# Kernel tuning notes

Measured on AMD Instinct MI355X. Metric: run time of the kernel, lower is better.

## Reference

```python
import jax, jax.numpy as jnp
import numpy as np

EPS = 1e-5

def _bn_relu(y, mean, var, scale, bias):
    # y: (b, c, n); eval-mode batchnorm over channel axis, then ReLU
    inv = scale / jnp.sqrt(var + EPS)
    return jax.nn.relu((y - mean[None, :, None]) * inv[None, :, None] + bias[None, :, None])

def setup_inputs() -> dict:
    key = jax.random.key(0)
    ks = jax.random.split(key, 6)
    b, c, n, cr = 4, 256, 4096, 32
    inp = {
        'x': jax.random.normal(ks[0], (b, c, n), jnp.float32),
        'w_q': jax.random.normal(ks[1], (cr, c), jnp.float32) * (1.0 / np.sqrt(c)),
        'w_k': jax.random.normal(ks[2], (cr, c), jnp.float32) * (1.0 / np.sqrt(c)),
        'w_v': jax.random.normal(ks[3], (c, c), jnp.float32) * (1.0 / np.sqrt(c)),
        'bn1_scale': jnp.ones((cr,), jnp.float32), 'bn1_bias': jnp.zeros((cr,), jnp.float32),
        'bn1_mean': jnp.zeros((cr,), jnp.float32), 'bn1_var': jnp.ones((cr,), jnp.float32),
        'bn2_scale': jnp.ones((cr,), jnp.float32), 'bn2_bias': jnp.zeros((cr,), jnp.float32),
        'bn2_mean': jnp.zeros((cr,), jnp.float32), 'bn2_var': jnp.ones((cr,), jnp.float32),
        'bn3_scale': jnp.ones((c,), jnp.float32), 'bn3_bias': jnp.zeros((c,), jnp.float32),
        'bn3_mean': jnp.zeros((c,), jnp.float32), 'bn3_var': jnp.ones((c,), jnp.float32),
        'gamma': jax.random.normal(ks[4], (1,), jnp.float32),
    }
    return inp

def reference(x, w_q, w_k, w_v,
              bn1_scale, bn1_bias, bn1_mean, bn1_var,
              bn2_scale, bn2_bias, bn2_mean, bn2_var,
              bn3_scale, bn3_bias, bn3_mean, bn3_var,
              gamma):
    # x: (b, c, n). Original views as (b, c, n, 1) so width=1, height=n.
    b, c, n = x.shape
    # 1x1 conv == channel matmul, then BN+ReLU
    q = _bn_relu(jnp.einsum('oc,bcn->bon', w_q, x), bn1_mean, bn1_var, bn1_scale, bn1_bias)  # (b, c', n)
    k = _bn_relu(jnp.einsum('oc,bcn->bon', w_k, x), bn2_mean, bn2_var, bn2_scale, bn2_bias)  # (b, c', n)
    v = _bn_relu(jnp.einsum('oc,bcn->bon', w_v, x), bn3_mean, bn3_var, bn3_scale, bn3_bias)  # (b, c, n)
    # energy_H: (b, n, n) with -inf diagonal (self-attention along 'height')
    energy_h = jnp.einsum('bdi,bdj->bij', q, k)
    eye = jnp.eye(n, dtype=bool)
    energy_h = jnp.where(eye[None], -jnp.inf, energy_h)
    # energy_W: width=1 -> per-position self energy (b, n)
    energy_w = jnp.sum(q * k, axis=1)
    # softmax over concat of n H-logits and 1 W-logit
    att = jax.nn.softmax(jnp.concatenate([energy_h, energy_w[..., None]], axis=-1), axis=-1)  # (b, n, n+1)
    att_h = att[..., :n]        # (b, n, n), query i -> key j
    att_w = att[..., n]         # (b, n)
    out_h = jnp.einsum('bcj,bij->bci', v, att_h)   # aggregate values along height
    out_w = v * att_w[:, None, :]                  # width=1 self term
    out = gamma[0] * (out_h + out_w) + x
    return out
```

## Files before the change

kernel.cpp:

```cpp
#include <hip/hip_runtime.h>

#define Bb 4
#define Cc 256
#define Nn 4096
#define CR 32
#define EPS_BN 1e-5f
#define SHIFT2 28.853900817779268f
#define LOG2E  1.4426950408889634f
#define JSPLIT 4
#define JSL (Nn / JSPLIT)
#define TJ 64
#define NTILES (JSL / TJ)

typedef __attribute__((ext_vector_type(8))) short short8;
typedef __attribute__((ext_vector_type(4))) float f32x4;

__device__ inline unsigned int pk2(float a, float b) {
    __bf16 ha = (__bf16)a, hb = (__bf16)b;
    unsigned short ra = __builtin_bit_cast(unsigned short, ha);
    unsigned short rb = __builtin_bit_cast(unsigned short, hb);
    return ((unsigned int)rb << 16) | ra;
}
__device__ inline float blo(unsigned int u) { return __uint_as_float(u << 16); }
__device__ inline float bhi(unsigned int u) { return __uint_as_float(u & 0xffff0000u); }
__device__ inline float ex2(float x) { return __builtin_amdgcn_exp2f(x); }

__global__ __launch_bounds__(256) void prep_w(
    const float* __restrict__ wq, const float* __restrict__ wk,
    const float* __restrict__ wv, __bf16* __restrict__ Wf)
{
    const int r16 = blockIdx.x;
    const int tid = threadIdx.x;
#pragma unroll
    for (int ss = 0; ss < 2; ++ss) {
        int s = tid + ss * 256;
        int kc = s >> 6, lane = s & 63;
        int R = r16 * 16 + (lane & 15);
        const float* src = (R < 32) ? (wq + (size_t)R * Cc)
                         : (R < 64) ? (wk + (size_t)(R - 32) * Cc)
                                    : (wv + (size_t)(R - 64) * Cc);
        const float* p = src + kc * 32 + (lane >> 4) * 8;
        float4 a = *(const float4*)p;
        float4 c2 = *(const float4*)(p + 4);
        uint4 pk = { pk2(a.x,a.y), pk2(a.z,a.w), pk2(c2.x,c2.y), pk2(c2.z,c2.w) };
        *(uint4*)&Wf[(((size_t)r16 * 8 + kc) * 64 + lane) * 8] = pk;
    }
}

__global__ __launch_bounds__(256) void qkv_kernel(
    const float* __restrict__ x, const __bf16* __restrict__ Wf,
    const float* __restrict__ bn1s, const float* __restrict__ bn1b, const float* __restrict__ bn1m, const float* __restrict__ bn1v,
    const float* __restrict__ bn2s, const float* __restrict__ bn2b, const float* __restrict__ bn2m, const float* __restrict__ bn2v,
    const float* __restrict__ bn3s, const float* __restrict__ bn3b, const float* __restrict__ bn3m, const float* __restrict__ bn3v,
    __bf16* __restrict__ Qt, __bf16* __restrict__ Kt, __bf16* __restrict__ Vb)
{
    __shared__ __align__(16) float  sXf[4][32 * 40];
    __shared__ __align__(16) __bf16 sXt[4][2][32 * 40];
    __shared__ __align__(16) __bf16 oT[128 * 136];

    const int tid = threadIdx.x;
    const int n0 = blockIdx.x * 128, g = blockIdx.y, b = blockIdx.z;
    const int lane = tid & 63, w = tid >> 6;
    const int l15 = lane & 15, l4 = lane >> 4;
    const int nmt = (g == 0) ? 4 : 8;
    const int r16b = (g == 0) ? 0 : 4 + (g - 1) * 8;

    float*  sXfw  = &sXf[w][0];
    __bf16* sXtw0 = &sXt[w][0][0];
    __bf16* sXtw1 = &sXt[w][1][0];

    const int cr = lane >> 3, nq = lane & 7;
    const float* xbase = x + (size_t)(b * Cc + cr) * Nn + n0 + w * 32 + nq * 4;

    float4 xg[4];
#pragma unroll
    for (int it = 0; it < 4; ++it)
        xg[it] = *(const float4*)&xbase[(size_t)(it * 8) * Nn];

    f32x4 acc[8][2];
#pragma unroll
    for (int mt = 0; mt < 8; ++mt)
#pragma unroll
        for (int nt = 0; nt < 2; ++nt) acc[mt][nt] = (f32x4){0.f, 0.f, 0.f, 0.f};

    for (int kc = 0; kc < 8; ++kc) {
#pragma unroll
        for (int it = 0; it < 4; ++it)
            *(float4*)&sXfw[(it * 8 + cr) * 40 + nq * 4] = xg[it];

        if (kc + 1 < 8) {
#pragma unroll
            for (int it = 0; it < 4; ++it)
                xg[it] = *(const float4*)&xbase[(size_t)((kc + 1) * 32 + it * 8) * Nn];
        }

#pragma unroll
        for (int s = 0; s < 2; ++s) {
            int n = lane & 31, c0 = (lane >> 5) * 8 + s * 16;
            float h[8], lo[8];
#pragma unroll
            for (int j = 0; j < 8; ++j) {
                float v = sXfw[(c0 + j) * 40 + n];
                float hh = (float)(__bf16)v;
                h[j] = hh; lo[j] = v - hh;
            }
            uint4 H = { pk2(h[0],h[1]), pk2(h[2],h[3]), pk2(h[4],h[5]), pk2(h[6],h[7]) };
            uint4 L = { pk2(lo[0],lo[1]), pk2(lo[2],lo[3]), pk2(lo[4],lo[5]), pk2(lo[6],lo[7]) };
            *(uint4*)&sXtw0[n * 40 + c0] = H;
            *(uint4*)&sXtw1[n * 40 + c0] = L;
        }

        short8 bh[2], bl[2];
#pragma unroll
        for (int nt = 0; nt < 2; ++nt) {
            bh[nt] = *(const short8*)&sXtw0[(nt * 16 + l15) * 40 + l4 * 8];
            bl[nt] = *(const short8*)&sXtw1[(nt * 16 + l15) * 40 + l4 * 8];
        }
        short8 af[8];
#pragma unroll
        for (int mt = 0; mt < 8; ++mt)
            if (mt < nmt)
                af[mt] = *(const short8*)&Wf[(((size_t)(r16b + mt) * 8 + kc) * 64 + lane) * 8];
#pragma unroll
        for (int mt = 0; mt < 8; ++mt) {
            if (mt < nmt) {
#pragma unroll
                for (int nt = 0; nt < 2; ++nt) {
                    acc[mt][nt] = __builtin_amdgcn_mfma_f32_16x16x32_bf16(af[mt], bh[nt], acc[mt][nt], 0, 0, 0);
                    acc[mt][nt] = __builtin_amdgcn_mfma_f32_16x16x32_bf16(af[mt], bl[nt], acc[mt][nt], 0, 0, 0);
                }
            }
        }
    }

    if (g == 0) {
#pragma unroll
        for (int mt = 0; mt < 4; ++mt) {
            float scl[4], off[4];
#pragma unroll
            for (int r = 0; r < 4; ++r) {
                int R = mt * 16 + l4 * 4 + r;
                float s, o;
                if (R < 32) {
                    s = bn1s[R] * __frsqrt_rn(bn1v[R] + EPS_BN);
                    o = bn1b[R] - bn1m[R] * s;
                } else {
                    int row = R - 32;
                    s = bn2s[row] * __frsqrt_rn(bn2v[row] + EPS_BN);
                    o = bn2b[row] - bn2m[row] * s;
                    s *= LOG2E; o *= LOG2E;
                }
                scl[r] = s; off[r] = o;
            }
            __bf16* dst = (mt < 2) ? Qt : Kt;
            int d0 = (mt & 1) * 16 + l4 * 4;
#pragma unroll
            for (int nt = 0; nt < 2; ++nt) {
                f32x4 a = acc[mt][nt];
                float e0 = fmaxf(fmaf(a.x, scl[0], off[0]), 0.f);
                float e1 = fmaxf(fmaf(a.y, scl[1], off[1]), 0.f);
                float e2 = fmaxf(fmaf(a.z, scl[2], off[2]), 0.f);
                float e3 = fmaxf(fmaf(a.w, scl[3], off[3]), 0.f);
                uint2 p = { pk2(e0, e1), pk2(e2, e3) };
                int n = n0 + w * 32 + nt * 16 + l15;
                *(uint2*)&dst[(size_t)(b * Nn + n) * CR + d0] = p;
            }
        }
    } else {
        const int vr0 = (g - 1) * 128;
#pragma unroll
        for (int mt = 0; mt < 8; ++mt) {
            float scl[4], off[4];
#pragma unroll
            for (int r = 0; r < 4; ++r) {
                int row = vr0 + mt * 16 + l4 * 4 + r;
                float s = bn3s[row] * __frsqrt_rn(bn3v[row] + EPS_BN);
                scl[r] = s; off[r] = bn3b[row] - bn3m[row] * s;
            }
#pragma unroll
            for (int nt = 0; nt < 2; ++nt) {
                f32x4 a = acc[mt][nt];
                float e[4];
                e[0] = fmaxf(fmaf(a.x, scl[0], off[0]), 0.f);
                e[1] = fmaxf(fmaf(a.y, scl[1], off[1]), 0.f);
                e[2] = fmaxf(fmaf(a.z, scl[2], off[2]), 0.f);
                e[3] = fmaxf(fmaf(a.w, scl[3], off[3]), 0.f);
                int ncol = w * 32 + nt * 16 + l15;
#pragma unroll
                for (int r = 0; r < 4; ++r)
                    oT[(mt * 16 + l4 * 4 + r) * 136 + ncol] = (__bf16)e[r];
            }
        }
        __syncthreads();
        int rr = tid >> 1, qq = tid & 1;
        size_t vrow = (size_t)(b * Cc + vr0 + rr) * Nn + n0 + qq * 64;
#pragma unroll
        for (int e8 = 0; e8 < 8; ++e8)
            *(uint4*)&Vb[vrow + e8 * 8] = *(const uint4*)&oT[rr * 136 + qq * 64 + e8 * 8];
    }
}

__global__ __launch_bounds__(256, 4) void attn_kernel(
    const __bf16* __restrict__ Qt, const __bf16* __restrict__ Kt,
    const __bf16* __restrict__ Vb,
    __bf16* __restrict__ PO, float* __restrict__ PL)
{
    __shared__ __align__(16) __bf16 sQ[64 * 40];
    __shared__ __align__(16) __bf16 sP[64 * 72];
    __shared__ __align__(16) float  sL[4][64];

    const int tid = threadIdx.x, lane = tid & 63, w = tid >> 6;
    const int b = blockIdx.z, iblk = blockIdx.x;
    const int js = blockIdx.y & 3, ch = blockIdx.y >> 2;
    const int i0 = iblk * 64, cb = ch * 128;
    const int l15 = lane & 15, l4 = lane >> 4;

    {
        int i = tid >> 2, o = tid & 3;
        *(uint4*)&sQ[i * 40 + o * 8] =
            *(const uint4*)&Qt[(size_t)(b * Nn + i0 + i) * CR + o * 8];
    }
    __syncthreads();
    short8 qf[4];
#pragma unroll
    for (int it = 0; it < 4; ++it)
        qf[it] = *(const short8*)&sQ[(it * 16 + l15) * 40 + l4 * 8];

    f32x4 oacc[8];
#pragma unroll
    for (int z = 0; z < 8; ++z) oacc[z] = (f32x4){0.f, 0.f, 0.f, 0.f};
    float lp[4] = {0.f, 0.f, 0.f, 0.f};

    const size_t jb = (size_t)js * JSL;
    short8 kf = *(const short8*)&Kt[(size_t)(b * Nn + jb + 16 * w + l15) * CR + l4 * 8];

    const __bf16* vrow0 = Vb + (size_t)(b * Cc + cb + w * 32 + l15) * Nn;

    for (int t = 0; t < NTILES; ++t) {
        const size_t j0 = jb + (size_t)t * TJ;

        short8 vf[4];
#pragma unroll
        for (int u = 0; u < 4; ++u) {
            int jh = u >> 1, ct = u & 1;
            vf[u] = *(const short8*)&vrow0[(size_t)(ct * 16) * Nn + j0 + jh * 32 + l4 * 8];
        }

#pragma unroll
        for (int it = 0; it < 4; ++it) {
            f32x4 c0 = (f32x4){0.f, 0.f, 0.f, 0.f};
            c0 = __builtin_amdgcn_mfma_f32_16x16x32_bf16(kf, qf[it], c0, 0, 0, 0);
            float e0 = ex2(c0.x - SHIFT2);
            float e1 = ex2(c0.y - SHIFT2);
            float e2 = ex2(c0.z - SHIFT2);
            float e3 = ex2(c0.w - SHIFT2);
            lp[it] += (e0 + e1) + (e2 + e3);
            uint2 p2 = { pk2(e0, e1), pk2(e2, e3) };
            *(uint2*)&sP[(it * 16 + l15) * 72 + w * 16 + l4 * 4] = p2;
        }
        __syncthreads();

        if (t + 1 < NTILES)
            kf = *(const short8*)&Kt[(size_t)(b * Nn + j0 + TJ + 16 * w + l15) * CR + l4 * 8];

        __builtin_amdgcn_s_setprio(1);
#pragma unroll
        for (int jh = 0; jh < 2; ++jh) {
            short8 pf[4];
#pragma unroll
            for (int it = 0; it < 4; ++it)
                pf[it] = *(const short8*)&sP[(it * 16 + l15) * 72 + jh * 32 + l4 * 8];
#pragma unroll
            for (int ct = 0; ct < 2; ++ct) {
#pragma unroll
                for (int it = 0; it < 4; ++it)
                    oacc[it * 2 + ct] = __builtin_amdgcn_mfma_f32_16x16x32_bf16(
                        pf[it], vf[jh * 2 + ct], oacc[it * 2 + ct], 0, 0, 0);
            }
        }
        __builtin_amdgcn_s_setprio(0);
        __syncthreads();
    }

#pragma unroll
    for (int it = 0; it < 4; ++it) {
        float v = lp[it];
        v += __shfl_xor(v, 16);
        v += __shfl_xor(v, 32);
        if (lane < 16) sL[w][it * 16 + lane] = v;
    }
    __syncthreads();
    if (ch == 0 && tid < 64)
        PL[(size_t)(js * Bb + b) * Nn + i0 + tid] =
            sL[0][tid] + sL[1][tid] + sL[2][tid] + sL[3][tid];

    const size_t base = (size_t)((js * Bb + b) * (Nn / 64) + iblk) * 16384;
#pragma unroll
    for (int it = 0; it < 4; ++it)
#pragma unroll
        for (int ct = 0; ct < 2; ++ct) {
            f32x4 a = oacc[it * 2 + ct];
            uint2 p = { pk2(a.x, a.y), pk2(a.z, a.w) };
            int g16 = ch * 8 + w * 2 + ct;
            int s = (g16 >> 2) * 16 + it * 4 + (g16 & 3);
            *(uint2*)&PO[base + (size_t)(s * 64 + lane) * 4] = p;
        }
}

__global__ __launch_bounds__(256) void reduce_kernel(
    const __bf16* __restrict__ PO, const float* __restrict__ PL,
    const float* __restrict__ x, const float* __restrict__ gamma,
    float* __restrict__ out)
{
    __shared__ __align__(16) float oT[64 * 68];
    __shared__ float sLinv[64];

    const int tid = threadIdx.x;
    const int iblk = blockIdx.x, wq = blockIdx.y, b = blockIdx.z;
    const int i0 = iblk * 64;
    const int lane = tid & 63, ct = tid >> 6, l15 = lane & 15, l4 = lane >> 4;

    if (tid < 64) {
        float l = 0.f;
#pragma unroll
        for (int js = 0; js < JSPLIT; ++js)
            l += PL[(size_t)(js * Bb + b) * Nn + i0 + tid];
        sLinv[tid] = 1.0f / l;
    }

    float o[4][4];
#pragma unroll
    for (int it = 0; it < 4; ++it) {
        o[it][0] = o[it][1] = o[it][2] = o[it][3] = 0.f;
#pragma unroll
        for (int js = 0; js < JSPLIT; ++js) {
            size_t base = (size_t)((js * Bb + b) * (Nn / 64) + iblk) * 16384;
            uint2 v = *(const uint2*)&PO[base + (size_t)((((wq * 4 + it) * 4 + ct) * 64 + lane)) * 4];
            o[it][0] += blo(v.x); o[it][1] += bhi(v.x);
            o[it][2] += blo(v.y); o[it][3] += bhi(v.y);
        }
    }

    const int cl = ct * 16 + l15;
#pragma unroll
    for (int it = 0; it < 4; ++it) {
        float4 t4 = { o[it][0], o[it][1], o[it][2], o[it][3] };
        *(float4*)&oT[cl * 68 + it * 16 + l4 * 4] = t4;
    }
    __syncthreads();

    const float g = gamma[0];
    const int c_l = tid >> 2, icol = (tid & 3) * 16;
    const int cg = wq * 64 + c_l;
    const size_t gb = (size_t)(b * Cc + cg) * Nn + i0 + icol;
#pragma unroll
    for (int k4 = 0; k4 < 4; ++k4) {
        float4 ov = *(const float4*)&oT[c_l * 68 + icol + k4 * 4];
        float4 li = *(const float4*)&sLinv[icol + k4 * 4];
        float4 xv = *(const float4*)&x[gb + k4 * 4];
        float4 res;
        res.x = fmaf(g, ov.x * li.x, xv.x);
        res.y = fmaf(g, ov.y * li.y, xv.y);
        res.z = fmaf(g, ov.z * li.z, xv.z);
        res.w = fmaf(g, ov.w * li.w, xv.w);
        *(float4*)&out[gb + k4 * 4] = res;
    }
}

extern "C" void kernel_launch(void* const* d_in, const int* in_sizes, int n_in,
                              void* d_out, int out_size, void* d_ws, size_t ws_size,
                              hipStream_t stream)
{
    const float* x    = (const float*)d_in[0];
    const float* wq   = (const float*)d_in[1];
    const float* wk   = (const float*)d_in[2];
    const float* wv   = (const float*)d_in[3];
    const float* bn1s = (const float*)d_in[4];
    const float* bn1b = (const float*)d_in[5];
    const float* bn1m = (const float*)d_in[6];
    const float* bn1v = (const float*)d_in[7];
    const float* bn2s = (const float*)d_in[8];
    const float* bn2b = (const float*)d_in[9];
    const float* bn2m = (const float*)d_in[10];
    const float* bn2v = (const float*)d_in[11];
    const float* bn3s = (const float*)d_in[12];
    const float* bn3b = (const float*)d_in[13];
    const float* bn3m = (const float*)d_in[14];
    const float* bn3v = (const float*)d_in[15];
    const float* gmm  = (const float*)d_in[16];
    float* out = (float*)d_out;

    char* ws = (char*)d_ws;
    __bf16* Qt  = (__bf16*)(ws);
    __bf16* Kt  = (__bf16*)(ws + (1u << 20));
    __bf16* Vb  = (__bf16*)(ws + (2u << 20));
    char*   big = ws + (10u << 20);
    __bf16* PO  = (__bf16*)big;
    float*  PL  = (float*)(big + 33554432);
    __bf16* Wf  = (__bf16*)(big + 33554432 + 262144);

    prep_w<<<dim3(20), 256, 0, stream>>>(wq, wk, wv, Wf);

    qkv_kernel<<<dim3(Nn / 128, 3, Bb), 256, 0, stream>>>(
        x, Wf,
        bn1s, bn1b, bn1m, bn1v,
        bn2s, bn2b, bn2m, bn2v,
        bn3s, bn3b, bn3m, bn3v,
        Qt, Kt, Vb);

    attn_kernel<<<dim3(Nn / 64, JSPLIT * 2, Bb), 256, 0, stream>>>(Qt, Kt, Vb, PO, PL);

    reduce_kernel<<<dim3(Nn / 64, 4, Bb), 256, 0, stream>>>(PO, PL, x, gmm, out);
}
```

Baseline: 209.8 us.

## Fuse split-K attention reduction into attention kernel with full-J loop per block

Removes the JSPLIT split of the key dimension and the separate reduce kernel. Each block now handles 32 queries across all 4096 keys and all 256 channels, normalises by the row sum and writes gamma*out + x directly. This drops the bf16 partial-output round trip through global memory and one kernel launch. In exchange the grid shrinks from 4096 to 512 blocks, each running a four-times-longer serial loop and reading all V rows per tile, so V reuse drops and occupancy/latency hiding may suffer.

```diff
diff --git a/kernel.cpp b/kernel.cpp
--- a/kernel.cpp
+++ b/kernel.cpp
@@ -7,10 +7,8 @@
 #define EPS_BN 1e-5f
 #define SHIFT2 28.853900817779268f
 #define LOG2E  1.4426950408889634f
-#define JSPLIT 4
-#define JSL (Nn / JSPLIT)
 #define TJ 64
-#define NTILES (JSL / TJ)
+#define NTJ (Nn / TJ)
 
 typedef __attribute__((ext_vector_type(8))) short short8;
 typedef __attribute__((ext_vector_type(4))) float f32x4;
@@ -21,8 +19,6 @@
     unsigned short rb = __builtin_bit_cast(unsigned short, hb);
     return ((unsigned int)rb << 16) | ra;
 }
-__device__ inline float blo(unsigned int u) { return __uint_as_float(u << 16); }
-__device__ inline float bhi(unsigned int u) { return __uint_as_float(u & 0xffff0000u); }
 __device__ inline float ex2(float x) { return __builtin_amdgcn_exp2f(x); }
 
 __global__ __launch_bounds__(256) void prep_w(
@@ -200,54 +196,54 @@
     }
 }
 
-__global__ __launch_bounds__(256, 4) void attn_kernel(
+__global__ __launch_bounds__(256) void attn_kernel(
     const __bf16* __restrict__ Qt, const __bf16* __restrict__ Kt,
     const __bf16* __restrict__ Vb,
-    __bf16* __restrict__ PO, float* __restrict__ PL)
+    const float* __restrict__ x, const float* __restrict__ gamma,
+    float* __restrict__ out)
 {
-    __shared__ __align__(16) __bf16 sQ[64 * 40];
-    __shared__ __align__(16) __bf16 sP[64 * 72];
-    __shared__ __align__(16) float  sL[4][64];
+    __shared__ __align__(16) __bf16 sQ[32 * 40];
+    __shared__ __align__(16) __bf16 sP[32 * 72];
+    __shared__ __align__(16) float  sL[4][32];
+    __shared__ __align__(16) float  sLinv[32];
+    __shared__ __align__(16) float  oT[256 * 36];
 
     const int tid = threadIdx.x, lane = tid & 63, w = tid >> 6;
-    const int b = blockIdx.z, iblk = blockIdx.x;
-    const int js = blockIdx.y & 3, ch = blockIdx.y >> 2;
-    const int i0 = iblk * 64, cb = ch * 128;
+    const int b = blockIdx.y, iblk = blockIdx.x;
+    const int i0 = iblk * 32;
     const int l15 = lane & 15, l4 = lane >> 4;
 
-    {
+    if (tid < 128) {
         int i = tid >> 2, o = tid & 3;
         *(uint4*)&sQ[i * 40 + o * 8] =
             *(const uint4*)&Qt[(size_t)(b * Nn + i0 + i) * CR + o * 8];
     }
     __syncthreads();
-    short8 qf[4];
-#pragma unroll
-    for (int it = 0; it < 4; ++it)
+    short8 qf[2];
+#pragma unroll
+    for (int it = 0; it < 2; ++it)
         qf[it] = *(const short8*)&sQ[(it * 16 + l15) * 40 + l4 * 8];
 
     f32x4 oacc[8];
 #pragma unroll
     for (int z = 0; z < 8; ++z) oacc[z] = (f32x4){0.f, 0.f, 0.f, 0.f};
-    float lp[4] = {0.f, 0.f, 0.f, 0.f};
-
-    const size_t jb = (size_t)js * JSL;
-    short8 kf = *(const short8*)&Kt[(size_t)(b * Nn + jb + 16 * w + l15) * CR + l4 * 8];
-
-    const __bf16* vrow0 = Vb + (size_t)(b * Cc + cb + w * 32 + l15) * Nn;
-
-    for (int t = 0; t < NTILES; ++t) {
-        const size_t j0 = jb + (size_t)t * TJ;
-
-        short8 vf[4];
-#pragma unroll
-        for (int u = 0; u < 4; ++u) {
-            int jh = u >> 1, ct = u & 1;
-            vf[u] = *(const short8*)&vrow0[(size_t)(ct * 16) * Nn + j0 + jh * 32 + l4 * 8];
-        }
-
-#pragma unroll
-        for (int it = 0; it < 4; ++it) {
+    float lp[2] = {0.f, 0.f};
+
+    short8 kf = *(const short8*)&Kt[(size_t)(b * Nn + 16 * w + l15) * CR + l4 * 8];
+
+    for (int t = 0; t < NTJ; ++t) {
+        const size_t j0 = (size_t)t * TJ;
+
+        short8 vf[8];
+#pragma unroll
+        for (int u = 0; u < 8; ++u) {
+            int jh = u >> 2, ct = u & 3;
+            int c = w * 64 + ct * 16 + l15;
+            vf[u] = *(const short8*)&Vb[(size_t)(b * Cc + c) * Nn + j0 + (jh * 4 + l4) * 8];
+        }
+
+#pragma unroll
+        for (int it = 0; it < 2; ++it) {
             f32x4 c0 = (f32x4){0.f, 0.f, 0.f, 0.f};
             c0 = __builtin_amdgcn_mfma_f32_16x16x32_bf16(kf, qf[it], c0, 0, 0, 0);
             float e0 = ex2(c0.x - SHIFT2);
@@ -260,22 +256,22 @@
         }
         __syncthreads();
 
-        if (t + 1 < NTILES)
+        if (t + 1 < NTJ)
             kf = *(const short8*)&Kt[(size_t)(b * Nn + j0 + TJ + 16 * w + l15) * CR + l4 * 8];
 
         __builtin_amdgcn_s_setprio(1);
 #pragma unroll
         for (int jh = 0; jh < 2; ++jh) {
-            short8 pf[4];
-#pragma unroll
-            for (int it = 0; it < 4; ++it)
+            short8 pf[2];
+#pragma unroll
+            for (int it = 0; it < 2; ++it)
                 pf[it] = *(const short8*)&sP[(it * 16 + l15) * 72 + jh * 32 + l4 * 8];
 #pragma unroll
-            for (int ct = 0; ct < 2; ++ct) {
-#pragma unroll
-                for (int it = 0; it < 4; ++it)
-                    oacc[it * 2 + ct] = __builtin_amdgcn_mfma_f32_16x16x32_bf16(
-                        pf[it], vf[jh * 2 + ct], oacc[it * 2 + ct], 0, 0, 0);
+            for (int ct = 0; ct < 4; ++ct) {
+#pragma unroll
+                for (int it = 0; it < 2; ++it)
+                    oacc[it * 4 + ct] = __builtin_amdgcn_mfma_f32_16x16x32_bf16(
+                        pf[it], vf[jh * 4 + ct], oacc[it * 4 + ct], 0, 0, 0);
             }
         }
         __builtin_amdgcn_s_setprio(0);
@@ -283,87 +279,46 @@
     }
 
 #pragma unroll
-    for (int it = 0; it < 4; ++it) {
+    for (int it = 0; it < 2; ++it) {
         float v = lp[it];
         v += __shfl_xor(v, 16);
         v += __shfl_xor(v, 32);
         if (lane < 16) sL[w][it * 16 + lane] = v;
     }
     __syncthreads();
-    if (ch == 0 && tid < 64)
-        PL[(size_t)(js * Bb + b) * Nn + i0 + tid] =
-            sL[0][tid] + sL[1][tid] + sL[2][tid] + sL[3][tid];
-
-    const size_t base = (size_t)((js * Bb + b) * (Nn / 64) + iblk) * 16384;
-#pragma unroll
-    for (int it = 0; it < 4; ++it)
-#pragma unroll
-        for (int ct = 0; ct < 2; ++ct) {
-            f32x4 a = oacc[it * 2 + ct];
-            uint2 p = { pk2(a.x, a.y), pk2(a.z, a.w) };
-            int g16 = ch * 8 + w * 2 + ct;
-            int s = (g16 >> 2) * 16 + it * 4 + (g16 & 3);
-            *(uint2*)&PO[base + (size_t)(s * 64 + lane) * 4] = p;
-        }
-}
-
-__global__ __launch_bounds__(256) void reduce_kernel(
-    const __bf16* __restrict__ PO, const float* __restrict__ PL,
-    const float* __restrict__ x, const float* __restrict__ gamma,
-    float* __restrict__ out)
-{
-    __shared__ __align__(16) float oT[64 * 68];
-    __shared__ float sLinv[64];
-
-    const int tid = threadIdx.x;
-    const int iblk = blockIdx.x, wq = blockIdx.y, b = blockIdx.z;
-    const int i0 = iblk * 64;
-    const int lane = tid & 63, ct = tid >> 6, l15 = lane & 15, l4 = lane >> 4;
-
-    if (tid < 64) {
-        float l = 0.f;
-#pragma unroll
-        for (int js = 0; js < JSPLIT; ++js)
-            l += PL[(size_t)(js * Bb + b) * Nn + i0 + tid];
-        sLinv[tid] = 1.0f / l;
-    }
-
-    float o[4][4];
-#pragma unroll
-    for (int it = 0; it < 4; ++it) {
-        o[it][0] = o[it][1] = o[it][2] = o[it][3] = 0.f;
-#pragma unroll
-        for (int js = 0; js < JSPLIT; ++js) {
-            size_t base = (size_t)((js * Bb + b) * (Nn / 64) + iblk) * 16384;
-            uint2 v = *(const uint2*)&PO[base + (size_t)((((wq * 4 + it) * 4 + ct) * 64 + lane)) * 4];
-            o[it][0] += blo(v.x); o[it][1] += bhi(v.x);
-            o[it][2] += blo(v.y); o[it][3] += bhi(v.y);
-        }
-    }
-
-    const int cl = ct * 16 + l15;
-#pragma unroll
-    for (int it = 0; it < 4; ++it) {
-        float4 t4 = { o[it][0], o[it][1], o[it][2], o[it][3] };
-        *(float4*)&oT[cl * 68 + it * 16 + l4 * 4] = t4;
-    }
+    if (tid < 32)
+        sLinv[tid] = 1.0f / (sL[0][tid] + sL[1][tid] + sL[2][tid] + sL[3][tid]);
     __syncthreads();
 
+#pragma unroll
+    for (int it = 0; it < 2; ++it) {
+        float4 li = *(const float4*)&sLinv[it * 16 + l4 * 4];
+#pragma unroll
+        for (int ct = 0; ct < 4; ++ct) {
+            f32x4 a = oacc[it * 4 + ct];
+            int c = w * 64 + ct * 16 + l15;
+            float4 tv = { a.x * li.x, a.y * li.y, a.z * li.z, a.w * li.w };
+            *(float4*)&oT[c * 36 + it * 16 + l4 * 4] = tv;
+        }
+    }
+    __syncthreads();
+
     const float g = gamma[0];
-    const int c_l = tid >> 2, icol = (tid & 3) * 16;
-    const int cg = wq * 64 + c_l;
-    const size_t gb = (size_t)(b * Cc + cg) * Nn + i0 + icol;
-#pragma unroll
-    for (int k4 = 0; k4 < 4; ++k4) {
-        float4 ov = *(const float4*)&oT[c_l * 68 + icol + k4 * 4];
-        float4 li = *(const float4*)&sLinv[icol + k4 * 4];
-        float4 xv = *(const float4*)&x[gb + k4 * 4];
-        float4 res;
-        res.x = fmaf(g, ov.x * li.x, xv.x);
-        res.y = fmaf(g, ov.y * li.y, xv.y);
-        res.z = fmaf(g, ov.z * li.z, xv.z);
-        res.w = fmaf(g, ov.w * li.w, xv.w);
-        *(float4*)&out[gb + k4 * 4] = res;
+#pragma unroll
+    for (int rep = 0; rep < 2; ++rep) {
+        int c_l = (tid >> 1) + rep * 128, icol = (tid & 1) * 16;
+        size_t gb = (size_t)(b * Cc + c_l) * Nn + i0 + icol;
+#pragma unroll
+        for (int k4 = 0; k4 < 4; ++k4) {
+            float4 ov = *(const float4*)&oT[c_l * 36 + icol + k4 * 4];
+            float4 xv = *(const float4*)&x[gb + k4 * 4];
+            float4 res;
+            res.x = fmaf(g, ov.x, xv.x);
+            res.y = fmaf(g, ov.y, xv.y);
+            res.z = fmaf(g, ov.z, xv.z);
+            res.w = fmaf(g, ov.w, xv.w);
+            *(float4*)&out[gb + k4 * 4] = res;
+        }
     }
 }
 
@@ -394,10 +349,7 @@
     __bf16* Qt  = (__bf16*)(ws);
     __bf16* Kt  = (__bf16*)(ws + (1u << 20));
     __bf16* Vb  = (__bf16*)(ws + (2u << 20));
-    char*   big = ws + (10u << 20);
-    __bf16* PO  = (__bf16*)big;
-    float*  PL  = (float*)(big + 33554432);
-    __bf16* Wf  = (__bf16*)(big + 33554432 + 262144);
+    __bf16* Wf  = (__bf16*)(ws + (10u << 20));
 
     prep_w<<<dim3(20), 256, 0, stream>>>(wq, wk, wv, Wf);
 
@@ -408,7 +360,5 @@
         bn3s, bn3b, bn3m, bn3v,
         Qt, Kt, Vb);
 
-    attn_kernel<<<dim3(Nn / 64, JSPLIT * 2, Bb), 256, 0, stream>>>(Qt, Kt, Vb, PO, PL);
-
-    reduce_kernel<<<dim3(Nn / 64, 4, Bb), 256, 0, stream>>>(PO, PL, x, gmm, out);
-}
+    attn_kernel<<<dim3(Nn / 32, Bb), 256, 0, stream>>>(Qt, Kt, Vb, x, gmm, out);
+}
```

After: 257.0 us. +22.5%, slower.

## Merge channel halves into one 512-thread attention block with 128-wide key tiles

Applied to the files above, without the earlier changes.

Each attention block now runs 8 waves covering all 256 value channels, instead of two blocks each handling 128 channels. This removes the duplicated QK^T MFMA and exp work that both channel-half blocks used to do. The key tile grows to 128 and the key split drops from 4 to 2, which halves the partial outputs written and later reduced. V fragment loads are software-pipelined across the four 32-column sub-steps. In exchange there are fewer, larger blocks with higher LDS and register pressure per block, and a longer serial loop per block.

```diff
diff --git a/kernel.cpp b/kernel.cpp
--- a/kernel.cpp
+++ b/kernel.cpp
@@ -7,9 +7,9 @@
 #define EPS_BN 1e-5f
 #define SHIFT2 28.853900817779268f
 #define LOG2E  1.4426950408889634f
-#define JSPLIT 4
+#define JSPLIT 2
 #define JSL (Nn / JSPLIT)
-#define TJ 64
+#define TJ 128
 #define NTILES (JSL / TJ)
 
 typedef __attribute__((ext_vector_type(8))) short short8;
@@ -200,31 +200,26 @@
     }
 }
 
-__global__ __launch_bounds__(256, 4) void attn_kernel(
+__global__ __launch_bounds__(512) void attn_kernel(
     const __bf16* __restrict__ Qt, const __bf16* __restrict__ Kt,
     const __bf16* __restrict__ Vb,
     __bf16* __restrict__ PO, float* __restrict__ PL)
 {
     __shared__ __align__(16) __bf16 sQ[64 * 40];
-    __shared__ __align__(16) __bf16 sP[64 * 72];
-    __shared__ __align__(16) float  sL[4][64];
+    __shared__ __align__(16) __bf16 sP[64 * 136];
+    __shared__ __align__(16) float  sL[8][64];
 
     const int tid = threadIdx.x, lane = tid & 63, w = tid >> 6;
-    const int b = blockIdx.z, iblk = blockIdx.x;
-    const int js = blockIdx.y & 3, ch = blockIdx.y >> 2;
-    const int i0 = iblk * 64, cb = ch * 128;
+    const int b = blockIdx.z, js = blockIdx.y, iblk = blockIdx.x;
+    const int i0 = iblk * 64;
     const int l15 = lane & 15, l4 = lane >> 4;
 
-    {
+    if (tid < 256) {
         int i = tid >> 2, o = tid & 3;
         *(uint4*)&sQ[i * 40 + o * 8] =
             *(const uint4*)&Qt[(size_t)(b * Nn + i0 + i) * CR + o * 8];
     }
     __syncthreads();
-    short8 qf[4];
-#pragma unroll
-    for (int it = 0; it < 4; ++it)
-        qf[it] = *(const short8*)&sQ[(it * 16 + l15) * 40 + l4 * 8];
 
     f32x4 oacc[8];
 #pragma unroll
@@ -233,18 +228,23 @@
 
     const size_t jb = (size_t)js * JSL;
     short8 kf = *(const short8*)&Kt[(size_t)(b * Nn + jb + 16 * w + l15) * CR + l4 * 8];
-
-    const __bf16* vrow0 = Vb + (size_t)(b * Cc + cb + w * 32 + l15) * Nn;
+    const __bf16* vrow0 = Vb + (size_t)(b * Cc + w * 32 + l15) * Nn;
 
     for (int t = 0; t < NTILES; ++t) {
         const size_t j0 = jb + (size_t)t * TJ;
 
-        short8 vf[4];
-#pragma unroll
-        for (int u = 0; u < 4; ++u) {
-            int jh = u >> 1, ct = u & 1;
-            vf[u] = *(const short8*)&vrow0[(size_t)(ct * 16) * Nn + j0 + jh * 32 + l4 * 8];
-        }
+        short8 v0[2], v1[2];
+#pragma unroll
+        for (int ct = 0; ct < 2; ++ct)
+            v0[ct] = *(const short8*)&vrow0[(size_t)(ct * 16) * Nn + j0 + l4 * 8];
+#pragma unroll
+        for (int ct = 0; ct < 2; ++ct)
+            v1[ct] = *(const short8*)&vrow0[(size_t)(ct * 16) * Nn + j0 + 32 + l4 * 8];
+
+        short8 qf[4];
+#pragma unroll
+        for (int it = 0; it < 4; ++it)
+            qf[it] = *(const short8*)&sQ[(it * 16 + l15) * 40 + l4 * 8];
 
 #pragma unroll
         for (int it = 0; it < 4; ++it) {
@@ -256,7 +256,7 @@
             float e3 = ex2(c0.w - SHIFT2);
             lp[it] += (e0 + e1) + (e2 + e3);
             uint2 p2 = { pk2(e0, e1), pk2(e2, e3) };
-            *(uint2*)&sP[(it * 16 + l15) * 72 + w * 16 + l4 * 4] = p2;
+            *(uint2*)&sP[(it * 16 + l15) * 136 + w * 16 + l4 * 4] = p2;
         }
         __syncthreads();
 
@@ -264,19 +264,59 @@
             kf = *(const short8*)&Kt[(size_t)(b * Nn + j0 + TJ + 16 * w + l15) * CR + l4 * 8];
 
         __builtin_amdgcn_s_setprio(1);
-#pragma unroll
-        for (int jh = 0; jh < 2; ++jh) {
+        {
             short8 pf[4];
 #pragma unroll
             for (int it = 0; it < 4; ++it)
-                pf[it] = *(const short8*)&sP[(it * 16 + l15) * 72 + jh * 32 + l4 * 8];
-#pragma unroll
-            for (int ct = 0; ct < 2; ++ct) {
+                pf[it] = *(const short8*)&sP[(it * 16 + l15) * 136 + l4 * 8];
+#pragma unroll
+            for (int ct = 0; ct < 2; ++ct)
 #pragma unroll
                 for (int it = 0; it < 4; ++it)
                     oacc[it * 2 + ct] = __builtin_amdgcn_mfma_f32_16x16x32_bf16(
-                        pf[it], vf[jh * 2 + ct], oacc[it * 2 + ct], 0, 0, 0);
-            }
+                        pf[it], v0[ct], oacc[it * 2 + ct], 0, 0, 0);
+        }
+#pragma unroll
+        for (int ct = 0; ct < 2; ++ct)
+            v0[ct] = *(const short8*)&vrow0[(size_t)(ct * 16) * Nn + j0 + 64 + l4 * 8];
+        {
+            short8 pf[4];
+#pragma unroll
+            for (int it = 0; it < 4; ++it)
+                pf[it] = *(const short8*)&sP[(it * 16 + l15) * 136 + 32 + l4 * 8];
+#pragma unroll
+            for (int ct = 0; ct < 2; ++ct)
+#pragma unroll
+                for (int it = 0; it < 4; ++it)
+                    oacc[it * 2 + ct] = __builtin_amdgcn_mfma_f32_16x16x32_bf16(
+                        pf[it], v1[ct], oacc[it * 2 + ct], 0, 0, 0);
+        }
+#pragma unroll
+        for (int ct = 0; ct < 2; ++ct)
+            v1[ct] = *(const short8*)&vrow0[(size_t)(ct * 16) * Nn + j0 + 96 + l4 * 8];
+        {
+            short8 pf[4];
+#pragma unroll
+            for (int it = 0; it < 4; ++it)
+                pf[it] = *(const short8*)&sP[(it * 16 + l15) * 136 + 64 + l4 * 8];
+#pragma unroll
+            for (int ct = 0; ct < 2; ++ct)
+#pragma unroll
+                for (int it = 0; it < 4; ++it)
+                    oacc[it * 2 + ct] = __builtin_amdgcn_mfma_f32_16x16x32_bf16(
+                        pf[it], v0[ct], oacc[it * 2 + ct], 0, 0, 0);
+        }
+        {
+            short8 pf[4];
+#pragma unroll
+            for (int it = 0; it < 4; ++it)
+                pf[it] = *(const short8*)&sP[(it * 16 + l15) * 136 + 96 + l4 * 8];
+#pragma unroll
+            for (int ct = 0; ct < 2; ++ct)
+#pragma unroll
+                for (int it = 0; it < 4; ++it)
+                    oacc[it * 2 + ct] = __builtin_amdgcn_mfma_f32_16x16x32_bf16(
+                        pf[it], v1[ct], oacc[it * 2 + ct], 0, 0, 0);
         }
         __builtin_amdgcn_s_setprio(0);
         __syncthreads();
@@ -290,9 +330,12 @@
         if (lane < 16) sL[w][it * 16 + lane] = v;
     }
     __syncthreads();
-    if (ch == 0 && tid < 64)
-        PL[(size_t)(js * Bb + b) * Nn + i0 + tid] =
-            sL[0][tid] + sL[1][tid] + sL[2][tid] + sL[3][tid];
+    if (tid < 64) {
+        float s = 0.f;
+#pragma unroll
+        for (int w8 = 0; w8 < 8; ++w8) s += sL[w8][tid];
+        PL[(size_t)(js * Bb + b) * Nn + i0 + tid] = s;
+    }
 
     const size_t base = (size_t)((js * Bb + b) * (Nn / 64) + iblk) * 16384;
 #pragma unroll
@@ -301,7 +344,7 @@
         for (int ct = 0; ct < 2; ++ct) {
             f32x4 a = oacc[it * 2 + ct];
             uint2 p = { pk2(a.x, a.y), pk2(a.z, a.w) };
-            int g16 = ch * 8 + w * 2 + ct;
+            int g16 = w * 2 + ct;
             int s = (g16 >> 2) * 16 + it * 4 + (g16 & 3);
             *(uint2*)&PO[base + (size_t)(s * 64 + lane) * 4] = p;
         }
@@ -408,7 +451,7 @@
         bn3s, bn3b, bn3m, bn3v,
         Qt, Kt, Vb);
 
-    attn_kernel<<<dim3(Nn / 64, JSPLIT * 2, Bb), 256, 0, stream>>>(Qt, Kt, Vb, PO, PL);
+    attn_kernel<<<dim3(Nn / 64, JSPLIT, Bb), 512, 0, stream>>>(Qt, Kt, Vb, PO, PL);
 
     reduce_kernel<<<dim3(Nn / 64, 4, Bb), 256, 0, stream>>>(PO, PL, x, gmm, out);
 }
```

Result: faster. 202.6 us (-3.4%).
